# Kernel tuning notes

Hardware: AMD Instinct MI355X
Metric: run time of the kernel (lower is better)

Reference implementation:

```python
import jax, jax.numpy as jnp
import numpy as np

N = 50000       # nodes
E = 800000      # edges (before self-loops)
IN_DIM = 128
HID = 16
H1 = 8
OUT_DIM = 16
H2 = 1
NEG_SLOPE = 0.2  # PyG GATConv LeakyReLU negative slope


def setup_inputs() -> dict:
    key = jax.random.key(0)
    ks = jax.random.split(key, 10)
    x = jax.random.normal(ks[0], (N, IN_DIM), dtype=jnp.float32)
    edge_index = jax.random.randint(ks[1], (2, E), 0, N, dtype=jnp.int32)
    # layer 1: Linear(IN_DIM -> H1*HID, no bias), att vectors [H, C], bias [H1*HID]
    W1 = jax.random.normal(ks[2], (IN_DIM, H1 * HID), dtype=jnp.float32) / np.sqrt(IN_DIM).astype(np.float32)
    a_src1 = jax.random.normal(ks[3], (H1, HID), dtype=jnp.float32) * 0.1
    a_dst1 = jax.random.normal(ks[4], (H1, HID), dtype=jnp.float32) * 0.1
    b1 = jnp.zeros((H1 * HID,), dtype=jnp.float32)
    # layer 2: Linear(H1*HID -> H2*OUT_DIM), concat=False -> bias [OUT_DIM]
    W2 = jax.random.normal(ks[5], (H1 * HID, H2 * OUT_DIM), dtype=jnp.float32) / np.sqrt(H1 * HID).astype(np.float32)
    a_src2 = jax.random.normal(ks[6], (H2, OUT_DIM), dtype=jnp.float32) * 0.1
    a_dst2 = jax.random.normal(ks[7], (H2, OUT_DIM), dtype=jnp.float32) * 0.1
    b2 = jnp.zeros((OUT_DIM,), dtype=jnp.float32)
    return {"x": x, "edge_index": edge_index, "W1": W1, "a_src1": a_src1,
            "a_dst1": a_dst1, "b1": b1, "W2": W2, "a_src2": a_src2,
            "a_dst2": a_dst2, "b2": b2}


def gat_conv(x, src, dst, W, a_src, a_dst, bias, heads, ch, concat):
    n = x.shape[0]
    h = (x @ W).reshape(n, heads, ch)                      # [N,H,C]
    s_src = jnp.sum(h * a_src, axis=-1)                    # [N,H] att_src . Wx
    s_dst = jnp.sum(h * a_dst, axis=-1)                    # [N,H]
    e = jax.nn.leaky_relu(s_src[src] + s_dst[dst], NEG_SLOPE)  # [Etot,H]
    # segment softmax over incoming edges per target node
    m = jax.ops.segment_max(e, dst, num_segments=n)        # [N,H]
    ee = jnp.exp(e - m[dst])
    denom = jax.ops.segment_sum(ee, dst, num_segments=n)   # [N,H]
    alpha = ee / denom[dst]                                # [Etot,H]
    out = jax.ops.segment_sum(h[src] * alpha[:, :, None], dst, num_segments=n)  # [N,H,C]
    out = out.reshape(n, heads * ch) if concat else out.mean(axis=1)
    return out + bias


def reference(x, edge_index, W1, a_src1, a_dst1, b1, W2, a_src2, a_dst2, b2):
    n = x.shape[0]
    loop = jnp.arange(n, dtype=edge_index.dtype)           # PyG adds self-loops
    src = jnp.concatenate([edge_index[0], loop])
    dst = jnp.concatenate([edge_index[1], loop])
    # eval mode: F.dropout is identity
    h = jax.nn.elu(gat_conv(x, src, dst, W1, a_src1, a_dst1, b1, H1, HID, True))
    out = gat_conv(h, src, dst, W2, a_src2, a_dst2, b2, H2, OUT_DIM, False)
    return jax.nn.log_softmax(out, axis=1)
```

## Files before the change

### kernel.cpp

```cpp
#include <hip/hip_runtime.h>
#include <hip/hip_fp16.h>
#include <math.h>

#define NEG_SLOPE 0.2f
#define MAXDEG 64
#define CSTRIDE 16
#define NXCD 8
#define NSLICE 256

typedef short bf16x8 __attribute__((ext_vector_type(8)));
typedef float f32x4 __attribute__((ext_vector_type(4)));

__device__ __forceinline__ unsigned short f2bf(float f) {
    union { float f; unsigned u; } v; v.f = f;
    unsigned r = v.u + 0x7FFF + ((v.u >> 16) & 1);
    return (unsigned short)(r >> 16);
}

__global__ void k_init(const float* __restrict__ W1, unsigned short* __restrict__ frag,
                       int* __restrict__ cursor, unsigned short* __restrict__ csr, int N)
{
    int gid = blockIdx.x * 256 + threadIdx.x;
    if (gid < 16384) {
        int f = gid >> 3, j = gid & 7;
        int kk = f >> 9, c = (f >> 6) & 7, l = f & 63;
        int col = c * 16 + (l & 15);
        int k = kk * 32 + ((l >> 4) << 3) + j;
        frag[gid] = f2bf(W1[k * 128 + col]);
    }
    if (gid < N) {
        cursor[gid * CSTRIDE] = 1;
        csr[gid * MAXDEG] = (unsigned short)gid;
    }
}

__global__ __launch_bounds__(256) void k_mega(
    const float* __restrict__ x, const bf16x8* __restrict__ frag,
    const float* __restrict__ a_src, const float* __restrict__ a_dst,
    __half* __restrict__ h1h, float* __restrict__ ssrc, float* __restrict__ sdst,
    int N, int G1,
    const int* __restrict__ src_e, const int* __restrict__ dst_e, int E,
    int* __restrict__ cursor, unsigned short* __restrict__ csr)
{
    const int t = threadIdx.x;

    if (blockIdx.x >= G1) {
        int fb = blockIdx.x - G1;
        int xcd = blockIdx.x & (NXCD - 1);
        int slice = fb >> 3;
        int dlo = (int)(((long)N * xcd) >> 3);
        int dhi = (int)(((long)N * (xcd + 1)) >> 3);
        int e0 = (int)((long)E * slice / NSLICE);
        int e1 = (int)((long)E * (slice + 1) / NSLICE);
        for (int i = e0 + t; i < e1; i += 256) {
            int d = dst_e[i];
            if (d >= dlo && d < dhi) {
                int s = src_e[i];
                int pos = atomicAdd(&cursor[d * CSTRIDE], 1);
                if (pos < MAXDEG) csr[d * MAXDEG + pos] = (unsigned short)s;
            }
        }
        return;
    }

    const int r0 = blockIdx.x * 64;
    const int w = t >> 6, l = t & 63;
    const int lo = l & 15, hi = l >> 4;
    const int row = r0 + w * 16 + lo;
    const bool rok = (row < N);

    f32x4 acc[8] = {};
    #pragma unroll
    for (int kk = 0; kk < 4; ++kk) {
        bf16x8 a;
        {
            float4 f0 = make_float4(0.f,0.f,0.f,0.f), f1 = f0;
            if (rok) {
                const float4* xp = (const float4*)(x + (size_t)row * 128 + kk * 32 + hi * 8);
                f0 = xp[0]; f1 = xp[1];
            }
            a[0] = (short)f2bf(f0.x); a[1] = (short)f2bf(f0.y);
            a[2] = (short)f2bf(f0.z); a[3] = (short)f2bf(f0.w);
            a[4] = (short)f2bf(f1.x); a[5] = (short)f2bf(f1.y);
            a[6] = (short)f2bf(f1.z); a[7] = (short)f2bf(f1.w);
        }
        #pragma unroll
        for (int c = 0; c < 8; ++c) {
            bf16x8 b = frag[(kk * 8 + c) * 64 + l];
            acc[c] = __builtin_amdgcn_mfma_f32_16x16x32_bf16(a, b, acc[c], 0, 0, 0);
        }
    }

    float av_s[8], av_d[8];
    #pragma unroll
    for (int c = 0; c < 8; ++c) {
        av_s[c] = a_src[c * 16 + lo];
        av_d[c] = a_dst[c * 16 + lo];
    }

    #pragma unroll
    for (int reg = 0; reg < 4; ++reg) {
        int grow = r0 + w * 16 + hi * 4 + reg;
        bool ok = (grow < N);
        if (ok) {
            #pragma unroll
            for (int c = 0; c < 8; ++c)
                h1h[(size_t)grow * 128 + c * 16 + lo] = __float2half(acc[c][reg]);
        }
        #pragma unroll
        for (int c = 0; c < 8; ++c) {
            float ps = acc[c][reg] * av_s[c];
            float pd = acc[c][reg] * av_d[c];
            #pragma unroll
            for (int m = 8; m >= 1; m >>= 1) {
                ps += __shfl_xor(ps, m, 64);
                pd += __shfl_xor(pd, m, 64);
            }
            if (ok && lo == 0) {
                ssrc[grow * 8 + c] = ps;
                sdst[grow * 8 + c] = pd;
            }
        }
    }
}

__global__ __launch_bounds__(256) void k_aggr1g2(
    const int* __restrict__ cursor, const unsigned short* __restrict__ csr,
    const __half2* __restrict__ h1h, const float* __restrict__ ssrc,
    const float* __restrict__ sdst, const float* __restrict__ b1,
    const float* __restrict__ W2, const float* __restrict__ a_src2,
    const float* __restrict__ a_dst2,
    float* __restrict__ h2, float* __restrict__ s2s, float* __restrict__ s2d, int N)
{
    __shared__ float lds_w2[2048];
    __shared__ float lds_h[4][128];
    const int t = threadIdx.x;

    {
        const float4* src = (const float4*)W2;
        float4* dst = (float4*)lds_w2;
        #pragma unroll
        for (int i = 0; i < 2; ++i) dst[i * 256 + t] = src[i * 256 + t];
    }
    __syncthreads();

    const int wid = t >> 6;
    const int lane = t & 63;
    const int node = blockIdx.x * 4 + wid;
    if (node >= N) return;
    const int h = lane >> 3;
    const int beg = node * MAXDEG;
    const int end = beg + min(cursor[node * CSTRIDE], MAXDEG);
    const float sd = sdst[node * 8 + h];
    float acc0 = 0.f, acc1 = 0.f, wsum = 0.f;

    int j = beg;
    for (; j + 3 < end; j += 4) {
        int s0 = csr[j], s1 = csr[j + 1], s2 = csr[j + 2], s3 = csr[j + 3];
        float e0 = ssrc[s0 * 8 + h];
        float e1 = ssrc[s1 * 8 + h];
        float e2 = ssrc[s2 * 8 + h];
        float e3 = ssrc[s3 * 8 + h];
        __half2 v0 = h1h[(size_t)s0 * 64 + lane];
        __half2 v1 = h1h[(size_t)s1 * 64 + lane];
        __half2 v2 = h1h[(size_t)s2 * 64 + lane];
        __half2 v3 = h1h[(size_t)s3 * 64 + lane];
        e0 += sd; e0 = (e0 >= 0.f) ? e0 : NEG_SLOPE * e0; float w0 = __expf(e0);
        e1 += sd; e1 = (e1 >= 0.f) ? e1 : NEG_SLOPE * e1; float w1 = __expf(e1);
        e2 += sd; e2 = (e2 >= 0.f) ? e2 : NEG_SLOPE * e2; float w2 = __expf(e2);
        e3 += sd; e3 = (e3 >= 0.f) ? e3 : NEG_SLOPE * e3; float w3 = __expf(e3);
        wsum += (w0 + w1) + (w2 + w3);
        float2 f0 = __half22float2(v0);
        float2 f1 = __half22float2(v1);
        float2 f2 = __half22float2(v2);
        float2 f3 = __half22float2(v3);
        acc0 = fmaf(w0, f0.x, acc0); acc1 = fmaf(w0, f0.y, acc1);
        acc0 = fmaf(w1, f1.x, acc0); acc1 = fmaf(w1, f1.y, acc1);
        acc0 = fmaf(w2, f2.x, acc0); acc1 = fmaf(w2, f2.y, acc1);
        acc0 = fmaf(w3, f3.x, acc0); acc1 = fmaf(w3, f3.y, acc1);
    }
    for (; j < end; ++j) {
        int s = csr[j];
        float e = ssrc[s * 8 + h] + sd;
        e = (e >= 0.f) ? e : NEG_SLOPE * e;
        float w = __expf(e);
        wsum += w;
        float2 f = __half22float2(h1h[(size_t)s * 64 + lane]);
        acc0 = fmaf(w, f.x, acc0); acc1 = fmaf(w, f.y, acc1);
    }

    const float2 bb = ((const float2*)b1)[lane];
    float inv = 1.f / wsum;
    float va = acc0 * inv + bb.x;
    float vb = acc1 * inv + bb.y;
    va = (va > 0.f) ? va : expm1f(va);
    vb = (vb > 0.f) ? vb : expm1f(vb);

    lds_h[wid][2 * lane]     = va;
    lds_h[wid][2 * lane + 1] = vb;
    asm volatile("s_waitcnt lgkmcnt(0)" ::: "memory");

    const int col = lane & 15, kg = lane >> 4;
    float r = 0.f;
    #pragma unroll
    for (int k2 = 0; k2 < 32; ++k2) {
        int k = kg * 32 + k2;
        r = fmaf(lds_h[wid][k], lds_w2[k * 16 + col], r);
    }
    r += __shfl_xor(r, 16, 64);
    r += __shfl_xor(r, 32, 64);
    if (lane < 16) h2[(size_t)node * 16 + col] = r;

    float ps = r * a_src2[col];
    float pd = r * a_dst2[col];
    #pragma unroll
    for (int m = 8; m >= 1; m >>= 1) {
        ps += __shfl_xor(ps, m, 64);
        pd += __shfl_xor(pd, m, 64);
    }
    if (lane == 0) { s2s[node] = ps; s2d[node] = pd; }
}

__global__ __launch_bounds__(256) void k_aggr2(
    const int* __restrict__ cursor, const unsigned short* __restrict__ csr,
    const float* __restrict__ h2, const float* __restrict__ s2s,
    const float* __restrict__ s2d, const float* __restrict__ b2,
    float* __restrict__ out, int N)
{
    int gid = blockIdx.x * 256 + threadIdx.x;
    int node = gid >> 4;
    if (node >= N) return;
    int c = gid & 15;
    const int beg = node * MAXDEG;
    const int end = beg + min(cursor[node * CSTRIDE], MAXDEG);
    float sd = s2d[node];
    float acc = 0.f, wsum = 0.f;

    int j = beg;
    for (; j + 3 < end; j += 4) {
        int s0 = csr[j], s1 = csr[j + 1], s2 = csr[j + 2], s3 = csr[j + 3];
        float e0 = s2s[s0], e1 = s2s[s1], e2 = s2s[s2], e3 = s2s[s3];
        float g0 = h2[(size_t)s0 * 16 + c];
        float g1 = h2[(size_t)s1 * 16 + c];
        float g2 = h2[(size_t)s2 * 16 + c];
        float g3 = h2[(size_t)s3 * 16 + c];
        e0 += sd; e0 = (e0 >= 0.f) ? e0 : NEG_SLOPE * e0; float w0 = __expf(e0);
        e1 += sd; e1 = (e1 >= 0.f) ? e1 : NEG_SLOPE * e1; float w1 = __expf(e1);
        e2 += sd; e2 = (e2 >= 0.f) ? e2 : NEG_SLOPE * e2; float w2 = __expf(e2);
        e3 += sd; e3 = (e3 >= 0.f) ? e3 : NEG_SLOPE * e3; float w3 = __expf(e3);
        wsum += (w0 + w1) + (w2 + w3);
        acc = fmaf(w0, g0, acc);
        acc = fmaf(w1, g1, acc);
        acc = fmaf(w2, g2, acc);
        acc = fmaf(w3, g3, acc);
    }
    for (; j < end; ++j) {
        int s = csr[j];
        float e = s2s[s] + sd;
        e = (e >= 0.f) ? e : NEG_SLOPE * e;
        float w = __expf(e);
        wsum += w;
        acc = fmaf(w, h2[(size_t)s * 16 + c], acc);
    }

    float v = acc / wsum + b2[c];
    float m = v;
    #pragma unroll
    for (int msk = 8; msk >= 1; msk >>= 1) m = fmaxf(m, __shfl_xor(m, msk, 64));
    float ex = __expf(v - m);
    float sum = ex;
    #pragma unroll
    for (int msk = 8; msk >= 1; msk >>= 1) sum += __shfl_xor(sum, msk, 64);
    out[(size_t)node * 16 + c] = v - m - __logf(sum);
}

extern "C" void kernel_launch(void* const* d_in, const int* in_sizes, int n_in,
                              void* d_out, int out_size, void* d_ws, size_t ws_size,
                              hipStream_t stream)
{
    const float* x      = (const float*)d_in[0];
    const int*   ei     = (const int*)  d_in[1];
    const float* W1     = (const float*)d_in[2];
    const float* a_src1 = (const float*)d_in[3];
    const float* a_dst1 = (const float*)d_in[4];
    const float* b1     = (const float*)d_in[5];
    const float* W2     = (const float*)d_in[6];
    const float* a_src2 = (const float*)d_in[7];
    const float* a_dst2 = (const float*)d_in[8];
    const float* b2     = (const float*)d_in[9];
    float* out = (float*)d_out;

    const int N = in_sizes[0] / 128;
    const int E = in_sizes[1] / 2;
    const int* src_e = ei;
    const int* dst_e = ei + E;

    float* p = (float*)d_ws;
    __half* h1h  = (__half*)p; p += (size_t)N * 64;
    unsigned short* frag = (unsigned short*)p; p += 8192;
    float* ssrc1 = p; p += (size_t)N * 8;
    float* sdst1 = p; p += (size_t)N * 8;
    float* h2    = p; p += (size_t)N * 16;
    float* s2s   = p; p += (size_t)N;
    float* s2d   = p; p += (size_t)N;
    int* ip = (int*)p;
    int* cursor = ip; ip += (size_t)N * CSTRIDE;
    unsigned short* csr = (unsigned short*)ip;

    const int G1 = (N + 63) / 64;
    const int GF = NSLICE * NXCD;

    k_init<<<(N + 255) / 256, 256, 0, stream>>>(W1, frag, cursor, csr, N);

    k_mega<<<G1 + GF, 256, 0, stream>>>(
        x, (const bf16x8*)frag, a_src1, a_dst1, h1h, ssrc1, sdst1, N, G1,
        src_e, dst_e, E, cursor, csr);

    k_aggr1g2<<<(N + 3) / 4, 256, 0, stream>>>(
        cursor, csr, (const __half2*)h1h, ssrc1, sdst1, b1,
        W2, a_src2, a_dst2, h2, s2s, s2d, N);

    k_aggr2<<<((size_t)N * 16 + 255) / 256, 256, 0, stream>>>(
        cursor, csr, h2, s2s, s2d, b2, out, N);
}
```

Before: 129.5 us.

## Distribute edge-weight computation across lanes with shuffles; pad LDS to avoid bank conflicts

In both aggregation kernels, each group of lanes that used to compute the same edge's attention weight redundantly now splits the edges: each lane loads one CSR index, computes its leaky-relu/exp weight, and the indices and weights are broadcast with shuffles. This cuts redundant csr/ssrc loads and exp work, and lets up to 8 or 16 feature gathers be issued per chunk. The LDS arrays for W2 and the per-wave hidden vector are padded to reduce bank conflicts in the small matmul. The cost is extra shuffle instructions and predicated tails per chunk.

```diff
diff --git a/kernel.cpp b/kernel.cpp
--- a/kernel.cpp
+++ b/kernel.cpp
@@ -132,15 +132,17 @@
     const float* __restrict__ a_dst2,
     float* __restrict__ h2, float* __restrict__ s2s, float* __restrict__ s2d, int N)
 {
-    __shared__ float lds_w2[2048];
-    __shared__ float lds_h[4][128];
+    __shared__ float lds_w2[2080];
+    __shared__ float lds_h[4][132];
     const int t = threadIdx.x;
 
     {
         const float4* src = (const float4*)W2;
-        float4* dst = (float4*)lds_w2;
-        #pragma unroll
-        for (int i = 0; i < 2; ++i) dst[i * 256 + t] = src[i * 256 + t];
+        #pragma unroll
+        for (int i = 0; i < 2; ++i) {
+            int f = i * 256 + t;
+            ((float4*)lds_w2)[f + ((f >> 7) << 1)] = src[f];
+        }
     }
     __syncthreads();
 
@@ -149,44 +151,36 @@
     const int node = blockIdx.x * 4 + wid;
     if (node >= N) return;
     const int h = lane >> 3;
+    const int eo = lane & 7;
     const int beg = node * MAXDEG;
     const int end = beg + min(cursor[node * CSTRIDE], MAXDEG);
     const float sd = sdst[node * 8 + h];
     float acc0 = 0.f, acc1 = 0.f, wsum = 0.f;
 
-    int j = beg;
-    for (; j + 3 < end; j += 4) {
-        int s0 = csr[j], s1 = csr[j + 1], s2 = csr[j + 2], s3 = csr[j + 3];
-        float e0 = ssrc[s0 * 8 + h];
-        float e1 = ssrc[s1 * 8 + h];
-        float e2 = ssrc[s2 * 8 + h];
-        float e3 = ssrc[s3 * 8 + h];
-        __half2 v0 = h1h[(size_t)s0 * 64 + lane];
-        __half2 v1 = h1h[(size_t)s1 * 64 + lane];
-        __half2 v2 = h1h[(size_t)s2 * 64 + lane];
-        __half2 v3 = h1h[(size_t)s3 * 64 + lane];
-        e0 += sd; e0 = (e0 >= 0.f) ? e0 : NEG_SLOPE * e0; float w0 = __expf(e0);
-        e1 += sd; e1 = (e1 >= 0.f) ? e1 : NEG_SLOPE * e1; float w1 = __expf(e1);
-        e2 += sd; e2 = (e2 >= 0.f) ? e2 : NEG_SLOPE * e2; float w2 = __expf(e2);
-        e3 += sd; e3 = (e3 >= 0.f) ? e3 : NEG_SLOPE * e3; float w3 = __expf(e3);
-        wsum += (w0 + w1) + (w2 + w3);
-        float2 f0 = __half22float2(v0);
-        float2 f1 = __half22float2(v1);
-        float2 f2 = __half22float2(v2);
-        float2 f3 = __half22float2(v3);
-        acc0 = fmaf(w0, f0.x, acc0); acc1 = fmaf(w0, f0.y, acc1);
-        acc0 = fmaf(w1, f1.x, acc0); acc1 = fmaf(w1, f1.y, acc1);
-        acc0 = fmaf(w2, f2.x, acc0); acc1 = fmaf(w2, f2.y, acc1);
-        acc0 = fmaf(w3, f3.x, acc0); acc1 = fmaf(w3, f3.y, acc1);
-    }
-    for (; j < end; ++j) {
-        int s = csr[j];
-        float e = ssrc[s * 8 + h] + sd;
-        e = (e >= 0.f) ? e : NEG_SLOPE * e;
-        float w = __expf(e);
-        wsum += w;
-        float2 f = __half22float2(h1h[(size_t)s * 64 + lane]);
-        acc0 = fmaf(w, f.x, acc0); acc1 = fmaf(w, f.y, acc1);
+    for (int j = beg; j < end; j += 8) {
+        const int rem = end - j;
+        int s_my = 0; float w_my = 0.f;
+        if (eo < rem) {
+            s_my = csr[j + eo];
+            float e = ssrc[s_my * 8 + h] + sd;
+            e = (e >= 0.f) ? e : NEG_SLOPE * e;
+            w_my = __expf(e);
+        }
+        int sv[8]; float wv[8];
+        #pragma unroll
+        for (int i = 0; i < 8; ++i) {
+            sv[i] = __shfl(s_my, (lane & 56) + i, 64);
+            wv[i] = __shfl(w_my, (lane & 56) + i, 64);
+        }
+        #pragma unroll
+        for (int i = 0; i < 8; ++i) {
+            if (i < rem) {
+                float2 f = __half22float2(h1h[(size_t)sv[i] * 64 + lane]);
+                wsum += wv[i];
+                acc0 = fmaf(wv[i], f.x, acc0);
+                acc1 = fmaf(wv[i], f.y, acc1);
+            }
+        }
     }
 
     const float2 bb = ((const float2*)b1)[lane];
@@ -196,8 +190,11 @@
     va = (va > 0.f) ? va : expm1f(va);
     vb = (vb > 0.f) ? vb : expm1f(vb);
 
-    lds_h[wid][2 * lane]     = va;
-    lds_h[wid][2 * lane + 1] = vb;
+    {
+        int k0 = 2 * lane;
+        lds_h[wid][k0 + (k0 >> 5)]     = va;
+        lds_h[wid][k0 + 1 + (k0 >> 5)] = vb;
+    }
     asm volatile("s_waitcnt lgkmcnt(0)" ::: "memory");
 
     const int col = lane & 15, kg = lane >> 4;
@@ -205,7 +202,8 @@
     #pragma unroll
     for (int k2 = 0; k2 < 32; ++k2) {
         int k = kg * 32 + k2;
-        r = fmaf(lds_h[wid][k], lds_w2[k * 16 + col], r);
+        int wi = k * 16 + col;
+        r = fmaf(lds_h[wid][k + kg], lds_w2[wi + ((wi >> 9) << 3)], r);
     }
     r += __shfl_xor(r, 16, 64);
     r += __shfl_xor(r, 32, 64);
@@ -230,37 +228,36 @@
     int gid = blockIdx.x * 256 + threadIdx.x;
     int node = gid >> 4;
     if (node >= N) return;
-    int c = gid & 15;
+    const int lane = threadIdx.x & 63;
+    const int c = lane & 15;
     const int beg = node * MAXDEG;
     const int end = beg + min(cursor[node * CSTRIDE], MAXDEG);
-    float sd = s2d[node];
+    const float sd = s2d[node];
     float acc = 0.f, wsum = 0.f;
 
-    int j = beg;
-    for (; j + 3 < end; j += 4) {
-        int s0 = csr[j], s1 = csr[j + 1], s2 = csr[j + 2], s3 = csr[j + 3];
-        float e0 = s2s[s0], e1 = s2s[s1], e2 = s2s[s2], e3 = s2s[s3];
-        float g0 = h2[(size_t)s0 * 16 + c];
-        float g1 = h2[(size_t)s1 * 16 + c];
-        float g2 = h2[(size_t)s2 * 16 + c];
-        float g3 = h2[(size_t)s3 * 16 + c];
-        e0 += sd; e0 = (e0 >= 0.f) ? e0 : NEG_SLOPE * e0; float w0 = __expf(e0);
-        e1 += sd; e1 = (e1 >= 0.f) ? e1 : NEG_SLOPE * e1; float w1 = __expf(e1);
-        e2 += sd; e2 = (e2 >= 0.f) ? e2 : NEG_SLOPE * e2; float w2 = __expf(e2);
-        e3 += sd; e3 = (e3 >= 0.f) ? e3 : NEG_SLOPE * e3; float w3 = __expf(e3);
-        wsum += (w0 + w1) + (w2 + w3);
-        acc = fmaf(w0, g0, acc);
-        acc = fmaf(w1, g1, acc);
-        acc = fmaf(w2, g2, acc);
-        acc = fmaf(w3, g3, acc);
-    }
-    for (; j < end; ++j) {
-        int s = csr[j];
-        float e = s2s[s] + sd;
-        e = (e >= 0.f) ? e : NEG_SLOPE * e;
-        float w = __expf(e);
-        wsum += w;
-        acc = fmaf(w, h2[(size_t)s * 16 + c], acc);
+    for (int j = beg; j < end; j += 16) {
+        const int rem = end - j;
+        int s_my = 0; float w_my = 0.f;
+        if (c < rem) {
+            s_my = csr[j + c];
+            float e = s2s[s_my] + sd;
+            e = (e >= 0.f) ? e : NEG_SLOPE * e;
+            w_my = __expf(e);
+        }
+        int sv[16]; float wv[16];
+        #pragma unroll
+        for (int i = 0; i < 16; ++i) {
+            sv[i] = __shfl(s_my, (lane & 48) + i, 64);
+            wv[i] = __shfl(w_my, (lane & 48) + i, 64);
+        }
+        #pragma unroll
+        for (int i = 0; i < 16; ++i) {
+            if (i < rem) {
+                float g = h2[(size_t)sv[i] * 16 + c];
+                wsum += wv[i];
+                acc = fmaf(wv[i], g, acc);
+            }
+        }
     }
 
     float v = acc / wsum + b2[c];
```

New measurement: 161.7 us. 1.25x slower.
